# Optimization experiments

Hardware: AMD Instinct MI355X
Metric: run time of the kernel (lower is better)

## Reference

```python
import jax, jax.numpy as jnp
import numpy as np

BETA = 0.25      # commitment loss weight
JSD_TS = 1.0     # softmax temperature


def _pairwise_sq_dist(x, cb):
    return (jnp.sum(x * x, axis=1, keepdims=True)
            + jnp.sum(cb * cb, axis=1)
            - 2.0 * jnp.matmul(x, cb.T))


def setup_inputs() -> dict:
    key = jax.random.key(0)
    k1, k2, k3 = jax.random.split(key, 3)
    B, D, H, W, K = 8, 512, 64, 64, 1024
    z = jax.random.normal(k1, (B, D, H, W), dtype=jnp.float32)
    z_pos = jax.random.normal(k2, (B, D, H, W), dtype=jnp.float32)
    # matches embedding.weight.data.uniform_(-1/K, 1/K)
    codebook = jax.random.uniform(k3, (K, D), dtype=jnp.float32,
                                  minval=-1.0 / K, maxval=1.0 / K)
    return {"z": z, "z_pos": z_pos, "codebook": codebook}


def reference(z, z_pos, codebook):
    b, d, h, w = z.shape
    # (b, d, h, w) -> (bhw, d)
    z_flat = jnp.transpose(z, (0, 2, 3, 1)).reshape(-1, d)
    z_pos_flat = jnp.transpose(z_pos, (0, 2, 3, 1)).reshape(-1, d)

    # normalize == 'none': z_norm = z_flat, codebook_norm = codebook
    dist = _pairwise_sq_dist(z_flat, codebook)          # (n, K)
    pos_dist = _pairwise_sq_dist(z_pos_flat, codebook)  # (n, K)

    min_encoding_indices = jnp.argmin(dist, axis=1)     # (n,)
    distance_prob = jax.nn.softmax(-dist / JSD_TS, axis=1)
    pos_distance_prob = jax.nn.softmax(-pos_dist / JSD_TS, axis=1)

    # use_weighted_sum == False: gather codebook rows
    z_q = codebook[min_encoding_indices]                # (n, d)

    codebook_loss = jnp.mean((z_q - jax.lax.stop_gradient(z_flat)) ** 2)
    commitment_loss = jnp.mean((z_flat - jax.lax.stop_gradient(z_q)) ** 2)
    q_loss = codebook_loss + BETA * commitment_loss

    # straight-through estimator
    z_q = z_flat + jax.lax.stop_gradient(z_q - z_flat)

    z_q = jnp.transpose(z_q.reshape(b, h, w, d), (0, 3, 1, 2))  # (b, d, h, w)
    return (z_q,
            q_loss,
            distance_prob.reshape(b, h, w, -1),
            min_encoding_indices.reshape(b, h, w),
            pos_distance_prob.reshape(b, h, w, -1))
```

## Files before the change

kernel.cpp:

```cpp
#include <hip/hip_runtime.h>
#include <hip/hip_bf16.h>

static constexpr int Bn = 8, Dn = 512, Hn = 64, Wn = 64, Kn = 1024;
static constexpr int HW = Hn * Wn;
static constexpr int NPIX = Bn * HW;
static constexpr size_t OFF_LOSS = (size_t)Bn * Dn * HW;
static constexpr size_t OFF_PROB = OFF_LOSS + 1;
static constexpr size_t OFF_IDX  = OFF_PROB + (size_t)NPIX * Kn;
static constexpr size_t OFF_PPRB = OFF_IDX + NPIX;

typedef __attribute__((ext_vector_type(8))) short short8v;
typedef __attribute__((ext_vector_type(4))) float f32x4;
typedef unsigned long long ull;
typedef unsigned int uint32;

static constexpr size_t WS_CB2   = 0;
static constexpr size_t WS_XXZ   = 4096;
static constexpr size_t WS_WIDX  = 135168;
static constexpr size_t WS_PART  = 266240;
static constexpr size_t WS_CBBF  = 282624;
static constexpr size_t WS_ABF   = 1331200;
static constexpr size_t ABF_BYTES = (size_t)2 * NPIX * Dn * 2;

#define MARGIN 1e-3f
#define CANDSLACK 2.5e-3f

__device__ inline unsigned short f2bf(float x) {
  unsigned u = __float_as_uint(x);
  u += 0x7fffu + ((u >> 16) & 1u);
  return (unsigned short)(u >> 16);
}
__device__ inline unsigned pack2(float a, float b) {
  return (unsigned)f2bf(a) | ((unsigned)f2bf(b) << 16);
}
__device__ inline float bf2f(unsigned short h) {
  return __uint_as_float(((unsigned)h) << 16);
}

__device__ inline void gload_lds16(const void* g, void* l) {
  __builtin_amdgcn_global_load_lds((const __attribute__((address_space(1))) void*)g,
                                   (__attribute__((address_space(3))) void*)l, 16, 0, 0);
}

__device__ float np_pairwise_sq512(const float* __restrict__ base, int stride) {
  float B[4];
#pragma unroll
  for (int blk = 0; blk < 4; blk++) {
    const float* a = base + (size_t)blk * 128 * stride;
    float r[8][4];
#pragma unroll
    for (int k = 0; k < 8; k++)
#pragma unroll
      for (int j = 0; j < 4; j++) {
        float x = a[(size_t)(4 * k + j) * stride];
        r[k][j] = __fmul_rn(x, x);
      }
#pragma unroll
    for (int i = 32; i < 128; i += 32)
#pragma unroll
      for (int k = 0; k < 8; k++)
#pragma unroll
        for (int j = 0; j < 4; j++) {
          float x = a[(size_t)(i + 4 * k + j) * stride];
          r[k][j] = __fadd_rn(r[k][j], __fmul_rn(x, x));
        }
    float L[4];
#pragma unroll
    for (int j = 0; j < 4; j++) {
      float t01 = __fadd_rn(r[0][j], r[1][j]);
      float t23 = __fadd_rn(r[2][j], r[3][j]);
      float t45 = __fadd_rn(r[4][j], r[5][j]);
      float t67 = __fadd_rn(r[6][j], r[7][j]);
      L[j] = __fadd_rn(__fadd_rn(t01, t23), __fadd_rn(t45, t67));
    }
    B[blk] = __fadd_rn(__fadd_rn(L[0], L[1]), __fadd_rn(L[2], L[3]));
  }
  return __fadd_rn(__fadd_rn(B[0], B[1]), __fadd_rn(B[2], B[3]));
}

__global__ __launch_bounds__(256) void k_init(const float* __restrict__ Z,
                                              const float* __restrict__ ZP,
                                              const float* __restrict__ CB,
                                              unsigned short* __restrict__ CBbf,
                                              unsigned short* __restrict__ Abf,
                                              float* __restrict__ xxZ,
                                              float* __restrict__ cb2) {
  int gid = blockIdx.x * 256 + threadIdx.x;
  {
    float2 f = *(const float2*)(CB + (size_t)gid * 2);
    union { __hip_bfloat162 h; unsigned u; } cv;
    cv.h = __float22bfloat162_rn(f);
    ((unsigned*)CBbf)[gid] = cv.u;
  }
  if (gid < 2 * NPIX) {
    const int p = gid & (NPIX - 1);
    const bool isz = gid < NPIX;
    const float* src = (isz ? Z : ZP) + (size_t)(p >> 12) * (Dn * HW) + (p & 4095);
    unsigned short* dst = Abf + (size_t)gid * Dn;
    float Bb[4];
#pragma unroll
    for (int blk = 0; blk < 4; blk++) {
      float rr[32];
#pragma unroll
      for (int i = 0; i < 128; i += 32) {
        float v[32];
#pragma unroll
        for (int t = 0; t < 32; t++) v[t] = src[(size_t)(blk * 128 + i + t) * HW];
        uint4 ua;
        unsigned* uw = (unsigned*)&ua;
#pragma unroll
        for (int q = 0; q < 4; q++) {
#pragma unroll
          for (int e = 0; e < 4; e++) uw[e] = pack2(v[q * 8 + 2 * e], v[q * 8 + 2 * e + 1]);
          *(uint4*)&dst[blk * 128 + i + q * 8] = ua;
        }
        if (isz) {
          if (i == 0) {
#pragma unroll
            for (int t = 0; t < 32; t++) rr[t] = __fmul_rn(v[t], v[t]);
          } else {
#pragma unroll
            for (int t = 0; t < 32; t++) rr[t] = __fadd_rn(rr[t], __fmul_rn(v[t], v[t]));
          }
        }
      }
      if (isz) {
        float L[4];
#pragma unroll
        for (int j = 0; j < 4; j++) {
          float t01 = __fadd_rn(rr[0 + j], rr[4 + j]);
          float t23 = __fadd_rn(rr[8 + j], rr[12 + j]);
          float t45 = __fadd_rn(rr[16 + j], rr[20 + j]);
          float t67 = __fadd_rn(rr[24 + j], rr[28 + j]);
          L[j] = __fadd_rn(__fadd_rn(t01, t23), __fadd_rn(t45, t67));
        }
        Bb[blk] = __fadd_rn(__fadd_rn(L[0], L[1]), __fadd_rn(L[2], L[3]));
      }
    }
    if (isz)
      xxZ[p] = __fadd_rn(__fadd_rn(Bb[0], Bb[1]), __fadd_rn(Bb[2], Bb[3]));
  } else if (gid < 2 * NPIX + Kn) {
    int k = gid - 2 * NPIX;
    cb2[k] = np_pairwise_sq512(CB + (size_t)k * Dn, 1);
  }
}

__global__ __launch_bounds__(256) void k_gemm(const unsigned short* __restrict__ Abf,
                                              const unsigned short* __restrict__ CBbf,
                                              const float* __restrict__ cb2,
                                              float* __restrict__ out) {
  __shared__ __align__(16) unsigned short sE[16384];
  __shared__ float c2s[128];
  __shared__ float rsv[2][128][2];
  __shared__ int   rsi[2][128];

  const int bid = blockIdx.x;
  const int kx = (bid >> 3) & 7;
  const int panel = (bid & 7) + 8 * (bid >> 6);
  const int py = panel & 255;
  const int zz = panel >> 8;
  const int p0 = py * 128;
  const int k0 = kx * 128;
  const unsigned short* Asrc = Abf + (size_t)((zz ? NPIX : 0) + p0) * Dn;
  float* Sf = out + (zz ? OFF_PPRB : OFF_PROB);
  uint32* Sg = (uint32*)Sf;

  const int tid = threadIdx.x;
  const int lane = tid & 63, w = tid >> 6;
  const int fr = lane & 15, fg = lane >> 4;
  const int wm = w & 1, wn = w >> 1;
  if (tid < 128) c2s[tid] = cb2[k0 + tid];

  auto stage = [&](int buf, int c0) {
#pragma unroll
    for (int h = 0; h < 2; h++) {
      const int G = tid + h * 256;
      const int row = G >> 2, g = G & 3;
      const int gsrc = g ^ ((row >> 1) & 3);
      const int ldsbase = ((tid & 192) + h * 256) * 8;
      gload_lds16(Asrc + (size_t)row * Dn + c0 + gsrc * 8, &sE[buf * 4096 + ldsbase]);
      gload_lds16(CBbf + (size_t)(k0 + row) * Dn + c0 + gsrc * 8,
                  &sE[8192 + buf * 4096 + ldsbase]);
    }
  };

  stage(0, 0);
  f32x4 acc[4][4] = {};
  const int swz = (fr >> 1) & 3;
#pragma unroll
  for (int s = 0; s < 16; s++) {
    __syncthreads();
    if (s < 15) stage((s + 1) & 1, (s + 1) * 32);
    const int cur = s & 1;
    short8v af[4], bf[4];
#pragma unroll
    for (int m = 0; m < 4; m++)
      af[m] = *(const short8v*)&sE[cur * 4096 + (wm * 64 + m * 16 + fr) * 32 + ((fg ^ swz) * 8)];
#pragma unroll
    for (int n = 0; n < 4; n++)
      bf[n] = *(const short8v*)&sE[8192 + cur * 4096 + (wn * 64 + n * 16 + fr) * 32 + ((fg ^ swz) * 8)];
#pragma unroll
    for (int m = 0; m < 4; m++)
#pragma unroll
      for (int n = 0; n < 4; n++)
        acc[m][n] = __builtin_amdgcn_mfma_f32_16x16x32_bf16(af[m], bf[n], acc[m][n], 0, 0, 0);
  }

  __syncthreads();
#pragma unroll
  for (int m = 0; m < 4; m++) {
#pragma unroll
    for (int r = 0; r < 4; r++) {
      const int px = wm * 64 + m * 16 + fg * 4 + r;
      float v1 = 1e30f, v2 = 1e30f;
      int i1 = 0x7fffffff;
#pragma unroll
      for (int n = 0; n < 4; n++) {
        const int kk = wn * 64 + n * 16 + fr;
        float sv = __fsub_rn(c2s[kk], __fmul_rn(2.0f, acc[m][n][r]));
        sE[px * 128 + (((kk >> 3) ^ (px & 15)) << 3) + (kk & 7)] = f2bf(sv);
        if (sv < v1) { v2 = v1; v1 = sv; i1 = kk; }
        else if (sv < v2) v2 = sv;
      }
#pragma unroll
      for (int d = 1; d < 16; d <<= 1) {
        float ov1 = __shfl_xor(v1, d, 64);
        int oi1 = __shfl_xor(i1, d, 64);
        float ov2 = __shfl_xor(v2, d, 64);
        float lose;
        if (ov1 < v1 || (ov1 == v1 && oi1 < i1)) { lose = v1; v1 = ov1; i1 = oi1; }
        else lose = ov1;
        v2 = fminf(fminf(v2, ov2), lose);
      }
      if (fr == 0) {
        rsv[wn][px][0] = v1; rsv[wn][px][1] = v2; rsi[wn][px] = i1;
      }
    }
  }
  __syncthreads();

  if (zz == 0 && tid < 128) {
    float v1 = rsv[0][tid][0], v2 = rsv[0][tid][1];
    int i1 = rsi[0][tid];
    float ov1 = rsv[1][tid][0], ov2 = rsv[1][tid][1];
    int oi1 = rsi[1][tid] + 64;
    oi1 = rsi[1][tid];
    float lose;
    if (ov1 < v1 || (ov1 == v1 && oi1 < i1)) { lose = v1; v1 = ov1; i1 = oi1; }
    else lose = ov1;
    v2 = fminf(fminf(v2, ov2), lose);
    float4 st;
    st.x = v1; st.y = v2; st.z = __int_as_float(k0 + i1); st.w = 0.f;
    *(float4*)(Sf + (size_t)(p0 + tid) * Kn + 512 + kx * 4) = st;
  }

  const int rr = tid >> 5;
  const int c32 = tid & 31;
#pragma unroll
  for (int pass = 0; pass < 16; pass++) {
    const int px = pass * 8 + rr;
    uint32* dst = Sg + (size_t)(p0 + px) * Kn + kx * 64;
#pragma unroll
    for (int i = 0; i < 2; i++) {
      const int w32 = c32 + 32 * i;
      const int kk2 = w32 * 2;
      const int g = kk2 >> 3;
      const int byteoff = px * 256 + ((g ^ (px & 15)) << 4) + (kk2 & 7) * 2;
      dst[w32] = *(const uint32*)((const char*)sE + byteoff);
    }
  }
}

__global__ __launch_bounds__(256) void k_row(const float* __restrict__ Z,
                                             const float* __restrict__ CB,
                                             const float* __restrict__ cb2,
                                             const float* __restrict__ xxZ,
                                             float* __restrict__ out,
                                             int* __restrict__ widx,
                                             float* __restrict__ partial) {
  __shared__ float lsum[4];
  const int zz = blockIdx.y;
  const int p0 = blockIdx.x * 16;
  float* Sbase = out + (zz ? OFF_PPRB : OFF_PROB);
  const int tid = threadIdx.x;
  const int lane = tid & 63, w = tid >> 6;
  float wloss = 0.f;

#pragma unroll 1
  for (int i = 0; i < 4; i++) {
    const int p = p0 + w * 4 + i;
    float* Sp = Sbase + (size_t)p * Kn;
    const uint32* Su = (const uint32*)Sp;
    uint32 uv[8];
#pragma unroll
    for (int q = 0; q < 8; q++) uv[q] = Su[q * 64 + lane];

    float sv[16];
    float sum = 0.f;
#pragma unroll
    for (int q = 0; q < 8; q++) {
      float s0 = bf2f((unsigned short)uv[q]);
      float s1 = bf2f((unsigned short)(uv[q] >> 16));
      sv[2 * q] = s0; sv[2 * q + 1] = s1;
      sum += __expf(-s0) + __expf(-s1);
    }
#pragma unroll
    for (int d = 1; d < 64; d <<= 1) sum += __shfl_xor(sum, d, 64);
    const float inv = 1.0f / sum;

    float v1 = 1e30f, v2 = 1e30f;
    int i1 = 0x7fffffff;
    if (zz == 0) {
      if (lane < 8) {
        float4 st = ((const float4*)(Sp + 512))[lane];
        v1 = st.x; v2 = st.y; i1 = __float_as_int(st.z);
      }
#pragma unroll
      for (int d = 1; d < 8; d <<= 1) {
        float ov1 = __shfl_xor(v1, d, 64);
        int oi1 = __shfl_xor(i1, d, 64);
        float ov2 = __shfl_xor(v2, d, 64);
        float lose;
        if (ov1 < v1 || (ov1 == v1 && oi1 < i1)) { lose = v1; v1 = ov1; i1 = oi1; }
        else lose = ov1;
        v2 = fminf(fminf(v2, ov2), lose);
      }
      v1 = __shfl(v1, 0, 64);
      v2 = __shfl(v2, 0, 64);
      i1 = __shfl(i1, 0, 64);
    }

#pragma unroll
    for (int q = 0; q < 8; q++) {
      int k0 = (q * 64 + lane) * 2;
      Sp[k0] = __expf(-sv[2 * q]) * inv;
      Sp[k0 + 1] = __expf(-sv[2 * q + 1]) * inv;
    }

    if (zz == 0) {
      int fin = i1;
      float dfin = v1;
      if (v2 <= v1 + MARGIN) {
        const float thrc = v1 + CANDSLACK;
        const float* zcol = Z + (size_t)(p >> 12) * (Dn * HW) + (p & 4095);
        float zc[8];
#pragma unroll
        for (int q = 0; q < 8; q++) zc[q] = zcol[(size_t)(lane + 64 * q) * HW];
        const float xx = xxZ[p];
        float bd = 1e30f;
        int bi = 0x7fffffff;
#pragma unroll
        for (int q = 0; q < 8; q++) {
#pragma unroll
          for (int hi = 0; hi < 2; hi++) {
            ull mask = __ballot(sv[2 * q + hi] <= thrc);
            while (mask) {
              int l = __ffsll(mask) - 1;
              mask &= mask - 1;
              int k = (q * 64 + l) * 2 + hi;
              const float* cr = CB + (size_t)k * Dn;
              float part = 0.f;
#pragma unroll
              for (int q2 = 0; q2 < 8; q2++)
                part = fmaf(zc[q2], cr[lane + 64 * q2], part);
#pragma unroll
              for (int d = 1; d < 64; d <<= 1) part += __shfl_xor(part, d, 64);
              float dd = __fsub_rn(__fadd_rn(xx, cb2[k]), __fmul_rn(2.0f, part));
              if (dd < bd || (dd == bd && k < bi)) { bd = dd; bi = k; }
            }
          }
        }
        fin = bi;
        dfin = bd - xx;
      }
      wloss += xxZ[p] + dfin;
      if (lane == 0) {
        widx[p] = fin;
        out[OFF_IDX + p] = (float)fin;
      }
    }
  }
  if (zz == 0) {
    if (lane == 0) lsum[w] = wloss;
    __syncthreads();
    if (tid == 0)
      partial[blockIdx.x] = (lsum[0] + lsum[1]) + (lsum[2] + lsum[3]);
  }
}

__global__ __launch_bounds__(256) void k_zq(const float* __restrict__ CB,
                                            const int* __restrict__ widx,
                                            float* __restrict__ out) {
  const int t = threadIdx.x;
  const size_t base = (size_t)blockIdx.x * 4096;
#pragma unroll
  for (int i = 0; i < 16; i++) {
    size_t e = base + (size_t)i * 256 + t;
    int hw = (int)(e & 4095);
    int c = (int)((e >> 12) & 511);
    int bb = (int)(e >> 21);
    int p = (bb << 12) | hw;
    out[e] = CB[(size_t)widx[p] * Dn + c];
  }
}

__global__ __launch_bounds__(256) void k_loss(const float* __restrict__ partial,
                                              float* __restrict__ out) {
  __shared__ float red[256];
  const int t = threadIdx.x;
  float s = 0.f;
  for (int i = t; i < 2048; i += 256) s += partial[i];
  red[t] = s;
  __syncthreads();
  for (int k = 128; k > 0; k >>= 1) {
    if (t < k) red[t] += red[t + k];
    __syncthreads();
  }
  if (t == 0) out[OFF_LOSS] = red[0] * (1.25f / 16777216.0f);
}

extern "C" void kernel_launch(void* const* d_in, const int* in_sizes, int n_in,
                              void* d_out, int out_size, void* d_ws, size_t ws_size,
                              hipStream_t stream) {
  const float* Z = (const float*)d_in[0];
  const float* ZP = (const float*)d_in[1];
  const float* CB = (const float*)d_in[2];
  float* out = (float*)d_out;
  char* ws = (char*)d_ws;
  float* cb2 = (float*)(ws + WS_CB2);
  float* xxZ = (float*)(ws + WS_XXZ);
  int* widx = (int*)(ws + WS_WIDX);
  float* partial = (float*)(ws + WS_PART);
  unsigned short* CBbf = (unsigned short*)(ws + WS_CBBF);
  unsigned short* Abf = (ws_size >= WS_ABF + ABF_BYTES)
                            ? (unsigned short*)(ws + WS_ABF)
                            : (unsigned short*)d_out;

  k_init<<<dim3(1024), 256, 0, stream>>>(Z, ZP, CB, CBbf, Abf, xxZ, cb2);
  k_gemm<<<dim3(4096), 256, 0, stream>>>(Abf, CBbf, cb2, out);
  k_row<<<dim3(2048, 2), 256, 0, stream>>>(Z, CB, cb2, xxZ, out, widx, partial);
  k_zq<<<dim3(4096), 256, 0, stream>>>(CB, widx, out);
  k_loss<<<dim3(1), 256, 0, stream>>>(partial, out);
}
```

Before: 419.9 us.

## Swap MFMA operand roles in GEMM epilogue and tile-transpose the z_q gather

```diff
diff --git a/kernel.cpp b/kernel.cpp
--- a/kernel.cpp
+++ b/kernel.cpp
@@ -192,49 +192,67 @@
     __syncthreads();
     if (s < 15) stage((s + 1) & 1, (s + 1) * 32);
     const int cur = s & 1;
-    short8v af[4], bf[4];
+    short8v kf[4], pf[4];
 #pragma unroll
     for (int m = 0; m < 4; m++)
-      af[m] = *(const short8v*)&sE[cur * 4096 + (wm * 64 + m * 16 + fr) * 32 + ((fg ^ swz) * 8)];
+      kf[m] = *(const short8v*)&sE[8192 + cur * 4096 + (wm * 64 + m * 16 + fr) * 32 + ((fg ^ swz) * 8)];
 #pragma unroll
     for (int n = 0; n < 4; n++)
-      bf[n] = *(const short8v*)&sE[8192 + cur * 4096 + (wn * 64 + n * 16 + fr) * 32 + ((fg ^ swz) * 8)];
+      pf[n] = *(const short8v*)&sE[cur * 4096 + (wn * 64 + n * 16 + fr) * 32 + ((fg ^ swz) * 8)];
 #pragma unroll
     for (int m = 0; m < 4; m++)
 #pragma unroll
       for (int n = 0; n < 4; n++)
-        acc[m][n] = __builtin_amdgcn_mfma_f32_16x16x32_bf16(af[m], bf[n], acc[m][n], 0, 0, 0);
+        acc[m][n] = __builtin_amdgcn_mfma_f32_16x16x32_bf16(kf[m], pf[n], acc[m][n], 0, 0, 0);
   }
 
   __syncthreads();
+  float v1a[4], v2a[4];
+  int i1a[4];
+#pragma unroll
+  for (int n = 0; n < 4; n++) { v1a[n] = 1e30f; v2a[n] = 1e30f; i1a[n] = 0x7fffffff; }
 #pragma unroll
   for (int m = 0; m < 4; m++) {
-#pragma unroll
-    for (int r = 0; r < 4; r++) {
-      const int px = wm * 64 + m * 16 + fg * 4 + r;
-      float v1 = 1e30f, v2 = 1e30f;
-      int i1 = 0x7fffffff;
-#pragma unroll
-      for (int n = 0; n < 4; n++) {
-        const int kk = wn * 64 + n * 16 + fr;
-        float sv = __fsub_rn(c2s[kk], __fmul_rn(2.0f, acc[m][n][r]));
-        sE[px * 128 + (((kk >> 3) ^ (px & 15)) << 3) + (kk & 7)] = f2bf(sv);
-        if (sv < v1) { v2 = v1; v1 = sv; i1 = kk; }
-        else if (sv < v2) v2 = sv;
-      }
-#pragma unroll
-      for (int d = 1; d < 16; d <<= 1) {
-        float ov1 = __shfl_xor(v1, d, 64);
-        int oi1 = __shfl_xor(i1, d, 64);
-        float ov2 = __shfl_xor(v2, d, 64);
-        float lose;
-        if (ov1 < v1 || (ov1 == v1 && oi1 < i1)) { lose = v1; v1 = ov1; i1 = oi1; }
-        else lose = ov1;
-        v2 = fminf(fminf(v2, ov2), lose);
-      }
-      if (fr == 0) {
-        rsv[wn][px][0] = v1; rsv[wn][px][1] = v2; rsi[wn][px] = i1;
-      }
+    const int kkb = wm * 64 + m * 16 + fg * 4;
+    const float4 c2v = *(const float4*)&c2s[kkb];
+#pragma unroll
+    for (int n = 0; n < 4; n++) {
+      const int px = wn * 64 + n * 16 + fr;
+      float s0 = __fsub_rn(c2v.x, __fmul_rn(2.0f, acc[m][n][0]));
+      float s1 = __fsub_rn(c2v.y, __fmul_rn(2.0f, acc[m][n][1]));
+      float s2 = __fsub_rn(c2v.z, __fmul_rn(2.0f, acc[m][n][2]));
+      float s3 = __fsub_rn(c2v.w, __fmul_rn(2.0f, acc[m][n][3]));
+      uint2 pk;
+      pk.x = pack2(s0, s1);
+      pk.y = pack2(s2, s3);
+      *(uint2*)((char*)sE + px * 256 + ((kkb * 2) ^ ((px & 15) << 4))) = pk;
+      if (s0 < v1a[n]) { v2a[n] = v1a[n]; v1a[n] = s0; i1a[n] = kkb; }
+      else if (s0 < v2a[n]) v2a[n] = s0;
+      if (s1 < v1a[n]) { v2a[n] = v1a[n]; v1a[n] = s1; i1a[n] = kkb + 1; }
+      else if (s1 < v2a[n]) v2a[n] = s1;
+      if (s2 < v1a[n]) { v2a[n] = v1a[n]; v1a[n] = s2; i1a[n] = kkb + 2; }
+      else if (s2 < v2a[n]) v2a[n] = s2;
+      if (s3 < v1a[n]) { v2a[n] = v1a[n]; v1a[n] = s3; i1a[n] = kkb + 3; }
+      else if (s3 < v2a[n]) v2a[n] = s3;
+    }
+  }
+#pragma unroll
+  for (int n = 0; n < 4; n++) {
+    float v1 = v1a[n], v2 = v2a[n];
+    int i1 = i1a[n];
+#pragma unroll
+    for (int d = 16; d < 64; d <<= 1) {
+      float ov1 = __shfl_xor(v1, d, 64);
+      int oi1 = __shfl_xor(i1, d, 64);
+      float ov2 = __shfl_xor(v2, d, 64);
+      float lose;
+      if (ov1 < v1 || (ov1 == v1 && oi1 < i1)) { lose = v1; v1 = ov1; i1 = oi1; }
+      else lose = ov1;
+      v2 = fminf(fminf(v2, ov2), lose);
+    }
+    if (fg == 0) {
+      const int px = wn * 64 + n * 16 + fr;
+      rsv[wm][px][0] = v1; rsv[wm][px][1] = v2; rsi[wm][px] = i1;
     }
   }
   __syncthreads();
@@ -243,8 +261,7 @@
     float v1 = rsv[0][tid][0], v2 = rsv[0][tid][1];
     int i1 = rsi[0][tid];
     float ov1 = rsv[1][tid][0], ov2 = rsv[1][tid][1];
-    int oi1 = rsi[1][tid] + 64;
-    oi1 = rsi[1][tid];
+    int oi1 = rsi[1][tid];
     float lose;
     if (ov1 < v1 || (ov1 == v1 && oi1 < i1)) { lose = v1; v1 = ov1; i1 = oi1; }
     else lose = ov1;
@@ -263,10 +280,7 @@
 #pragma unroll
     for (int i = 0; i < 2; i++) {
       const int w32 = c32 + 32 * i;
-      const int kk2 = w32 * 2;
-      const int g = kk2 >> 3;
-      const int byteoff = px * 256 + ((g ^ (px & 15)) << 4) + (kk2 & 7) * 2;
-      dst[w32] = *(const uint32*)((const char*)sE + byteoff);
+      dst[w32] = *(const uint32*)((const char*)sE + px * 256 + ((w32 * 4) ^ ((px & 15) << 4)));
     }
   }
 }
@@ -391,16 +405,32 @@
 __global__ __launch_bounds__(256) void k_zq(const float* __restrict__ CB,
                                             const int* __restrict__ widx,
                                             float* __restrict__ out) {
-  const int t = threadIdx.x;
-  const size_t base = (size_t)blockIdx.x * 4096;
-#pragma unroll
-  for (int i = 0; i < 16; i++) {
-    size_t e = base + (size_t)i * 256 + t;
-    int hw = (int)(e & 4095);
-    int c = (int)((e >> 12) & 511);
-    int bb = (int)(e >> 21);
-    int p = (bb << 12) | hw;
-    out[e] = CB[(size_t)widx[p] * Dn + c];
+  __shared__ float tile[64][65];
+  __shared__ int wl[64];
+  const int p0 = blockIdx.x * 64;
+  const int b = p0 >> 12, hw0 = p0 & 4095;
+  const int tid = threadIdx.x;
+  if (tid < 64) wl[tid] = widx[p0 + tid];
+  __syncthreads();
+  const int px = tid >> 2, q = tid & 3;
+  const int px2 = tid & 63, cg = tid >> 6;
+  float* obase = out + (size_t)b * (Dn * HW) + hw0;
+  for (int c0 = 0; c0 < 512; c0 += 64) {
+    const float4* src = (const float4*)(CB + (size_t)wl[px] * Dn + c0 + q * 16);
+#pragma unroll
+    for (int j = 0; j < 4; j++) {
+      float4 v = src[j];
+      int c = q * 16 + j * 4;
+      tile[c + 0][px] = v.x; tile[c + 1][px] = v.y;
+      tile[c + 2][px] = v.z; tile[c + 3][px] = v.w;
+    }
+    __syncthreads();
+#pragma unroll
+    for (int pass = 0; pass < 16; pass++) {
+      int c = pass * 4 + cg;
+      obase[(size_t)(c0 + c) * HW + px2] = tile[c][px2];
+    }
+    __syncthreads();
   }
 }
 
@@ -439,6 +469,6 @@
   k_init<<<dim3(1024), 256, 0, stream>>>(Z, ZP, CB, CBbf, Abf, xxZ, cb2);
   k_gemm<<<dim3(4096), 256, 0, stream>>>(Abf, CBbf, cb2, out);
   k_row<<<dim3(2048, 2), 256, 0, stream>>>(Z, CB, cb2, xxZ, out, widx, partial);
-  k_zq<<<dim3(4096), 256, 0, stream>>>(CB, widx, out);
+  k_zq<<<dim3(512), 256, 0, stream>>>(CB, widx, out);
   k_loss<<<dim3(1), 256, 0, stream>>>(partial, out);
 }
```

New measurement: 355.1 us. -15.4%, faster.
